# Optimization experiments

Hardware: AMD Instinct MI355X
Metric: run time of the kernel (lower is better)

Reference implementation:

```python
import jax, jax.numpy as jnp
import numpy as np

N_NODES = 20000
N_EDGES = 320000
IN_DIM = 256
OUT_DIM = 256
NUM_RELS = 8
NUM_BASES = 4


def setup_inputs() -> dict:
    key = jax.random.key(0)
    k = jax.random.split(key, 7)
    return {
        "h": jax.random.normal(k[0], (N_NODES, IN_DIM), dtype=jnp.float32),
        "basis": jax.random.normal(k[1], (NUM_BASES, IN_DIM, OUT_DIM), dtype=jnp.float32)
        * (6.0 / (IN_DIM + OUT_DIM)) ** 0.5,
        "w_comp": jax.random.normal(k[2], (NUM_RELS, NUM_BASES), dtype=jnp.float32),
        "bias": jax.random.normal(k[3], (OUT_DIM,), dtype=jnp.float32) * 0.01,
        "src": jax.random.randint(k[4], (N_EDGES,), 0, N_NODES, dtype=jnp.int32),
        "dst": jax.random.randint(k[5], (N_EDGES,), 0, N_NODES, dtype=jnp.int32),
        "etype": jax.random.randint(k[6], (N_EDGES,), 0, NUM_RELS, dtype=jnp.int32),
    }


def reference(h, basis, w_comp, bias, src, dst, etype):
    # Faithful to the torch basis-decomposition quirk:
    #   weight.view(in, B, out); matmul(w_comp, .) -> [in, R, out]; view -> [R, in, out]
    in_dim, out_dim = h.shape[1], basis.shape[2]
    num_rels = w_comp.shape[0]
    wr = basis.reshape(in_dim, NUM_BASES, out_dim)          # raw-buffer reinterpret (torch .view)
    weight = jnp.einsum("rb,ibo->iro", w_comp, wr)          # [in, R, out]
    weight = weight.reshape(num_rels, in_dim, out_dim)      # raw-buffer reinterpret (torch .view)

    # msg_e = h[src_e] @ weight[etype_e]. Group by relation: transform all nodes
    # under every relation weight (dense GEMMs), then gather per edge.
    t = jnp.einsum("nd,rdo->rno", h, weight)                # [R, N, out]
    msg = t[etype, src]                                     # [E, out]

    # scatter-sum aggregation to destination nodes (dgl fn.sum)
    agg = jax.ops.segment_sum(msg, dst, num_segments=h.shape[0])  # [N, out]
    return jax.nn.relu(agg + bias)
```

## Files before the change

kernel.cpp:

```cpp
#include <hip/hip_runtime.h>


#define N_NODES  20000
#define N_EDGES  320000
#define IN_DIM   256
#define OUT_DIM  256
#define NUM_RELS 8
#define KDIM     128
#define M_PAD    20032
#define SUBCAP   16

#define FOLD_BLOCKS 2500
#define FILL_BLOCKS 1250
#define BP_BLOCKS   128

typedef __attribute__((ext_vector_type(8)))  short short8;
typedef __attribute__((ext_vector_type(16))) float float16v;

static __device__ __forceinline__ unsigned f2bf_rne(float x) {
    unsigned u = __float_as_uint(x);
    return (u + 0x7fffu + ((u >> 16) & 1u)) >> 16;
}

__global__ __launch_bounds__(256)
void prep_kernel(const float* __restrict__ h, const float* __restrict__ w_comp,
                 unsigned short* __restrict__ U,
                 const int* __restrict__ src, const int* __restrict__ dst,
                 const int* __restrict__ et,
                 int* __restrict__ cnt2, unsigned short* __restrict__ bucket2,
                 const float* __restrict__ basis, unsigned short* __restrict__ Bp) {
    int b = blockIdx.x;
    int t = threadIdx.x;
    if (b < FOLD_BLOCKS) {
        int gid = b * 256 + t;
        int n = gid >> 5, k = gid & 31;
        const float* hp = h + (size_t)n * IN_DIM + k * 8;
        float4 h0 = *(const float4*)hp;
        float4 h1 = *(const float4*)(hp + 4);
        float hv[8] = {h0.x, h0.y, h0.z, h0.w, h1.x, h1.y, h1.z, h1.w};
        float a0 = 0.f, a1 = 0.f, a2 = 0.f, a3 = 0.f;
#pragma unroll
        for (int j = 0; j < 8; ++j) {
            float hj = hv[j];
            a0 += hj * w_comp[j * 4 + 0];
            a1 += hj * w_comp[j * 4 + 1];
            a2 += hj * w_comp[j * 4 + 2];
            a3 += hj * w_comp[j * 4 + 3];
        }
        uint2 p;
        p.x = f2bf_rne(a0) | (f2bf_rne(a1) << 16);
        p.y = f2bf_rne(a2) | (f2bf_rne(a3) << 16);
        *(uint2*)(U + ((size_t)n << 7) + k * 4) = p;
    } else if (b < FOLD_BLOCKS + FILL_BLOCKS) {
        int e = (b - FOLD_BLOCKS) * 256 + t;
        int g = dst[e] * 8 + et[e];
        int p = atomicAdd(&cnt2[g], 1);
        if (p < SUBCAP) bucket2[(g << 4) + p] = (unsigned short)src[e];
    } else {
        int frag = (b - FOLD_BLOCKS - FILL_BLOCKS) * 256 + t;
        int lane = frag & 63;
        int ks   = (frag >> 6) & 7;
        int r    = (frag >> 9) & 7;
        int ct   = frag >> 12;
        int o  = ct * 32 + (lane & 31);
        int kb = r * 128 + ks * 16 + (lane >> 5) * 8;
        const float* bsp = basis + (size_t)kb * 256 + o;
        unsigned v[8];
#pragma unroll
        for (int j = 0; j < 8; ++j) v[j] = f2bf_rne(bsp[(size_t)j * 256]);
        uint4 p;
        p.x = v[0] | (v[1] << 16);
        p.y = v[2] | (v[3] << 16);
        p.z = v[4] | (v[5] << 16);
        p.w = v[6] | (v[7] << 16);
        *(uint4*)(Bp + (size_t)frag * 8) = p;
    }
}

__global__ __launch_bounds__(256)
void aggregate_kernel(const unsigned short* __restrict__ U,
                      const int* __restrict__ cnt2,
                      const unsigned short* __restrict__ bucket2,
                      unsigned int* __restrict__ S) {
    int wid  = threadIdx.x >> 6;
    int lane = threadIdx.x & 63;
    int half = lane >> 5;
    int l32  = lane & 31;
    int d = blockIdx.x * 4 + wid;

    float4 acc[NUM_RELS];
#pragma unroll
    for (int r = 0; r < NUM_RELS; ++r) acc[r] = make_float4(0.f, 0.f, 0.f, 0.f);

    if (d < N_NODES) {
        int base = d * 8;
        int4 ca = *(const int4*)(cnt2 + base);
        int4 cb = *(const int4*)(cnt2 + base + 4);
        int c[8] = {ca.x, ca.y, ca.z, ca.w, cb.x, cb.y, cb.z, cb.w};
#pragma unroll
        for (int r = 0; r < 8; ++r) if (c[r] > SUBCAP) c[r] = SUBCAP;

        uint2 ga[8];
#pragma unroll
        for (int r = 0; r < 8; ++r) {
            int s = bucket2[((base + r) << 4) + half];
            ga[r] = *(const uint2*)(U + ((size_t)s << 7) + l32 * 4);
        }
#pragma unroll
        for (int r = 0; r < 8; ++r) {
            if (half < c[r]) {
                acc[r].x += __uint_as_float(ga[r].x << 16);
                acc[r].y += __uint_as_float(ga[r].x & 0xffff0000u);
                acc[r].z += __uint_as_float(ga[r].y << 16);
                acc[r].w += __uint_as_float(ga[r].y & 0xffff0000u);
            }
        }
#pragma unroll
        for (int r = 0; r < 8; ++r) {
            for (int i = 2; i < c[r]; i += 2) {
                int s = bucket2[((base + r) << 4) + i + half];
                uint2 g = *(const uint2*)(U + ((size_t)s << 7) + l32 * 4);
                if (i + half < c[r]) {
                    acc[r].x += __uint_as_float(g.x << 16);
                    acc[r].y += __uint_as_float(g.x & 0xffff0000u);
                    acc[r].z += __uint_as_float(g.y << 16);
                    acc[r].w += __uint_as_float(g.y & 0xffff0000u);
                }
            }
        }
    }
#pragma unroll
    for (int r = 0; r < NUM_RELS; ++r) {
        acc[r].x += __shfl_xor(acc[r].x, 32);
        acc[r].y += __shfl_xor(acc[r].y, 32);
        acc[r].z += __shfl_xor(acc[r].z, 32);
        acc[r].w += __shfl_xor(acc[r].w, 32);
    }
    if (half == 0) {
#pragma unroll
        for (int r = 0; r < NUM_RELS; ++r) {
            uint2 p;
            p.x = f2bf_rne(acc[r].x) | (f2bf_rne(acc[r].y) << 16);
            p.y = f2bf_rne(acc[r].z) | (f2bf_rne(acc[r].w) << 16);
            *(uint2*)(S + (((size_t)r * M_PAD + d) << 6) + l32 * 2) = p;
        }
    }
}

__global__ __launch_bounds__(512)
void gemm_kernel(const unsigned short* __restrict__ S,
                 const unsigned short* __restrict__ Bp,
                 const float* __restrict__ bias,
                 float* __restrict__ out) {
    __shared__ unsigned short At[32][136];
    int t = threadIdx.x;
    int w = t >> 6, lane = t & 63;
    int ln = lane & 31, hi = lane >> 5;
    int n0 = blockIdx.x * 32;
    int c0 = w * 32;

    int srow = t >> 4, sq = t & 15;
    const unsigned short* sbase = S + (((size_t)n0 + srow) << 7) + sq * 8;
    uint4 pre = *(const uint4*)sbase;

    float16v acc = {};

    for (int r = 0; r < NUM_RELS; ++r) {
        if (r > 0) __syncthreads();
        *(uint4*)&At[srow][sq * 8] = pre;
        __syncthreads();
        if (r + 1 < NUM_RELS)
            pre = *(const uint4*)(sbase + (((size_t)(r + 1) * M_PAD) << 7));
        const unsigned short* bpr = Bp + (((size_t)(w * 8 + r) * 8) << 9) + lane * 8;
#pragma unroll
        for (int ks = 0; ks < 8; ++ks) {
            short8 a  = *(const short8*)&At[ln][ks * 16 + hi * 8];
            short8 bo = *(const short8*)(bpr + (ks << 9));
            acc = __builtin_amdgcn_mfma_f32_32x32x16_bf16(a, bo, acc, 0, 0, 0);
        }
    }

    float bs = bias[c0 + ln];
#pragma unroll
    for (int reg = 0; reg < 16; ++reg) {
        int row = (reg & 3) + 8 * (reg >> 2) + 4 * hi;
        int n = n0 + row;
        if (n < N_NODES)
            out[(size_t)n * OUT_DIM + c0 + ln] = fmaxf(acc[reg] + bs, 0.f);
    }
}

extern "C" void kernel_launch(void* const* d_in, const int* in_sizes, int n_in,
                              void* d_out, int out_size, void* d_ws, size_t ws_size,
                              hipStream_t stream) {
    const float* h      = (const float*)d_in[0];
    const float* basis  = (const float*)d_in[1];
    const float* w_comp = (const float*)d_in[2];
    const float* bias   = (const float*)d_in[3];
    const int*   src    = (const int*)d_in[4];
    const int*   dst    = (const int*)d_in[5];
    const int*   etype  = (const int*)d_in[6];
    float*       out    = (float*)d_out;

    char* ws = (char*)d_ws;
    size_t off = 0;
    unsigned short* U   = (unsigned short*)(ws + off); off += (size_t)N_NODES * KDIM * 2;
    unsigned int*   S   = (unsigned int*)(ws + off);   off += (size_t)NUM_RELS * M_PAD * KDIM * 2;
    unsigned short* Bp  = (unsigned short*)(ws + off); off += (size_t)8 * 8 * 8 * 64 * 8 * 2;
    int* cnt2 = (int*)(ws + off); off += (size_t)M_PAD * 8 * 4;
    unsigned short* bucket2 = (unsigned short*)(ws + off);
    off += ((size_t)M_PAD * 8 * SUBCAP + 128) * 2;

    hipMemsetAsync(cnt2, 0, (size_t)N_NODES * 8 * 4, stream);

    prep_kernel<<<FOLD_BLOCKS + FILL_BLOCKS + BP_BLOCKS, 256, 0, stream>>>(
        h, w_comp, U, src, dst, etype, cnt2, bucket2, basis, Bp);

    aggregate_kernel<<<M_PAD / 4, 256, 0, stream>>>(U, cnt2, bucket2, S);

    gemm_kernel<<<M_PAD / 32, 512, 0, stream>>>((const unsigned short*)S, Bp, bias, out);
}
```

Before: 144.3 us.

## Write aggregated features in MFMA fragment order and drop LDS staging in GEMM

The aggregate kernel now stores its per-relation bf16 sums directly in the 32x32x16 MFMA A-fragment layout, grouped per 32-node tile. The GEMM then loads A fragments straight from global memory with contiguous 16-byte loads instead of staging through shared memory with barriers. It also prefetches the next relation's A and B fragments into registers while the current MFMAs run. This removes the LDS round trip and __syncthreads, but raises register pressure and makes the aggregate kernel's stores more scattered.

Result: slower. 162.0 us (+12.3%).

```diff
diff --git a/kernel.cpp b/kernel.cpp
--- a/kernel.cpp
+++ b/kernel.cpp
@@ -137,47 +137,58 @@
         acc[r].w += __shfl_xor(acc[r].w, 32);
     }
     if (half == 0) {
+        int g   = d >> 5;
+        int ks  = l32 >> 2;
+        int hi2 = (l32 >> 1) & 1;
+        int flane = (d & 31) + (hi2 << 5);
+        size_t u0 = ((((size_t)g << 3) << 3) + ks) << 8;
+        int addl = (flane << 2) + ((l32 & 1) << 1);
 #pragma unroll
         for (int r = 0; r < NUM_RELS; ++r) {
             uint2 p;
             p.x = f2bf_rne(acc[r].x) | (f2bf_rne(acc[r].y) << 16);
             p.y = f2bf_rne(acc[r].z) | (f2bf_rne(acc[r].w) << 16);
-            *(uint2*)(S + (((size_t)r * M_PAD + d) << 6) + l32 * 2) = p;
+            *(uint2*)(S + u0 + ((size_t)r << 11) + addl) = p;
         }
     }
 }
 
 __global__ __launch_bounds__(512)
-void gemm_kernel(const unsigned short* __restrict__ S,
+void gemm_kernel(const unsigned short* __restrict__ Sf,
                  const unsigned short* __restrict__ Bp,
                  const float* __restrict__ bias,
                  float* __restrict__ out) {
-    __shared__ unsigned short At[32][136];
     int t = threadIdx.x;
     int w = t >> 6, lane = t & 63;
     int ln = lane & 31, hi = lane >> 5;
-    int n0 = blockIdx.x * 32;
+    int g = blockIdx.x;
+    int n0 = g * 32;
     int c0 = w * 32;
 
-    int srow = t >> 4, sq = t & 15;
-    const unsigned short* sbase = S + (((size_t)n0 + srow) << 7) + sq * 8;
-    uint4 pre = *(const uint4*)sbase;
+    const unsigned short* ap = Sf + ((size_t)g << 15) + lane * 8;
+    const unsigned short* bp = Bp + ((size_t)w << 15) + lane * 8;
 
     float16v acc = {};
-
+    short8 a[8], b[8], an[8], bn[8];
+#pragma unroll
+    for (int ks = 0; ks < 8; ++ks) {
+        a[ks] = *(const short8*)(ap + ((size_t)ks << 9));
+        b[ks] = *(const short8*)(bp + ((size_t)ks << 9));
+    }
+#pragma unroll
     for (int r = 0; r < NUM_RELS; ++r) {
-        if (r > 0) __syncthreads();
-        *(uint4*)&At[srow][sq * 8] = pre;
-        __syncthreads();
-        if (r + 1 < NUM_RELS)
-            pre = *(const uint4*)(sbase + (((size_t)(r + 1) * M_PAD) << 7));
-        const unsigned short* bpr = Bp + (((size_t)(w * 8 + r) * 8) << 9) + lane * 8;
-#pragma unroll
-        for (int ks = 0; ks < 8; ++ks) {
-            short8 a  = *(const short8*)&At[ln][ks * 16 + hi * 8];
-            short8 bo = *(const short8*)(bpr + (ks << 9));
-            acc = __builtin_amdgcn_mfma_f32_32x32x16_bf16(a, bo, acc, 0, 0, 0);
-        }
+        if (r + 1 < NUM_RELS) {
+#pragma unroll
+            for (int ks = 0; ks < 8; ++ks) {
+                an[ks] = *(const short8*)(ap + ((size_t)((r + 1) * 8 + ks) << 9));
+                bn[ks] = *(const short8*)(bp + ((size_t)((r + 1) * 8 + ks) << 9));
+            }
+        }
+#pragma unroll
+        for (int ks = 0; ks < 8; ++ks)
+            acc = __builtin_amdgcn_mfma_f32_32x32x16_bf16(a[ks], b[ks], acc, 0, 0, 0);
+#pragma unroll
+        for (int ks = 0; ks < 8; ++ks) { a[ks] = an[ks]; b[ks] = bn[ks]; }
     }
 
     float bs = bias[c0 + ln];
```
